# Optimization experiments

Measured on AMD Instinct MI355X. Metric: run time of the kernel, lower is better.

Reference implementation:

```python
import jax, jax.numpy as jnp
import numpy as np

SIGMA = 0.4  # init kwarg: width of Gaussian band around diagonal


def setup_inputs() -> dict:
    key = jax.random.key(0)
    k1, k2, k3 = jax.random.split(key, 3)
    B, T_OUT, T_IN = 64, 2000, 512
    alignments = jax.random.uniform(k1, (B, T_OUT, T_IN), dtype=jnp.float32)
    # lengths in [T/2, T] to avoid degenerate zero-length sequences
    input_lengths = jax.random.randint(k2, (B,), T_IN // 2, T_IN + 1, dtype=jnp.int32)
    output_lengths = jax.random.randint(k3, (B,), T_OUT // 2, T_OUT + 1, dtype=jnp.int32)
    return {"alignments": alignments, "input_lengths": input_lengths,
            "output_lengths": output_lengths}


def reference(alignments, input_lengths, output_lengths):
    B, T_out, T_in = alignments.shape
    dt = alignments.dtype
    i = jnp.arange(T_out, dtype=dt)[None, :, None]          # [1, T_out, 1]
    j = jnp.arange(T_in, dtype=dt)[None, None, :]           # [1, 1, T_in]
    Ti = input_lengths.astype(dt)[:, None, None]            # [B, 1, 1]
    To = output_lengths.astype(dt)[:, None, None]           # [B, 1, 1]
    expected_j = j / Ti * To                                # diagonal target position
    w = 1.0 - jnp.exp(-((i - expected_j) ** 2) / (2.0 * SIGMA ** 2))
    # original loops only fill b,i<T_out[b], j<T_in[b]; rest stays zero
    valid = (i < To) & (j < Ti)
    w = jnp.where(valid, w, jnp.zeros((), dt))
    return jnp.sum(alignments * w) / B
```

## Files before the change

### kernel.cpp

```cpp
#include <hip/hip_runtime.h>


#define GAL_SIGMA 0.4f
#define GAL_TIN   512
#define GAL_BMAX  256

typedef float vfloat4 __attribute__((ext_vector_type(4)));

__global__ __launch_bounds__(256) void gal_main_kernel(
    const float* __restrict__ align,
    const int*   __restrict__ in_len,
    const int*   __restrict__ out_len,
    float*       __restrict__ partials,
    int n_rows, int T_out, int B)
{
    const int lane = threadIdx.x & 63;
    const int wid  = threadIdx.x >> 6;
    const int waves_total = gridDim.x << 2;
    const float cexp = -1.0f / (2.0f * GAL_SIGMA * GAL_SIGMA);

    __shared__ int   sTo[GAL_BMAX];
    __shared__ int   sTi[GAL_BMAX];
    __shared__ float sRatio[GAL_BMAX];
    for (int t = threadIdx.x; t < B && t < GAL_BMAX; t += 256) {
        const int ti = in_len[t];
        const int to = out_len[t];
        sTi[t] = ti; sTo[t] = to;
        sRatio[t] = (float)to / (float)ti;
    }
    __syncthreads();

    float acc = 0.0f;

    const int j0a = lane << 2;
    const int j0b = 256 + (lane << 2);

    for (int row = (blockIdx.x << 2) + wid; row < n_rows; row += waves_total) {
        const int b = row / T_out;
        const int i = row - b * T_out;
        const int To = (b < GAL_BMAX) ? sTo[b] : out_len[b];
        if (i >= To) continue;
        const int   Ti    = (b < GAL_BMAX) ? sTi[b]    : in_len[b];
        const float ratio = (b < GAL_BMAX) ? sRatio[b] : ((float)To / (float)Ti);
        const float fi    = (float)i;

        const vfloat4* rowp = (const vfloat4*)(align + (size_t)row * GAL_TIN);

        const bool v0 = j0a < Ti;
        const bool v1 = j0b < Ti;
        vfloat4 a0 = {0.f, 0.f, 0.f, 0.f}, a1 = {0.f, 0.f, 0.f, 0.f};
        if (v0) a0 = __builtin_nontemporal_load(rowp + lane);
        if (v1) a1 = __builtin_nontemporal_load(rowp + lane + 64);

        if (v0) {
            #pragma unroll
            for (int e = 0; e < 4; ++e) {
                const int j = j0a + e;
                const float d = fi - (float)j * ratio;
                const float w = 1.0f - __expf(d * d * cexp);
                acc += (j < Ti) ? a0[e] * w : 0.0f;
            }
        }
        if (v1) {
            #pragma unroll
            for (int e = 0; e < 4; ++e) {
                const int j = j0b + e;
                const float d = fi - (float)j * ratio;
                const float w = 1.0f - __expf(d * d * cexp);
                acc += (j < Ti) ? a1[e] * w : 0.0f;
            }
        }
    }

    #pragma unroll
    for (int off = 32; off > 0; off >>= 1)
        acc += __shfl_down(acc, off, 64);

    __shared__ float smem[4];
    if (lane == 0) smem[wid] = acc;
    __syncthreads();
    if (threadIdx.x == 0)
        partials[blockIdx.x] = smem[0] + smem[1] + smem[2] + smem[3];
}

__global__ __launch_bounds__(256) void gal_reduce_kernel(
    const float* __restrict__ partials,
    float*       __restrict__ out,
    int n, float inv_B)
{
    float acc = 0.0f;
    for (int idx = threadIdx.x; idx < n; idx += 256)
        acc += partials[idx];

    #pragma unroll
    for (int off = 32; off > 0; off >>= 1)
        acc += __shfl_down(acc, off, 64);

    __shared__ float smem[4];
    const int lane = threadIdx.x & 63;
    const int wid  = threadIdx.x >> 6;
    if (lane == 0) smem[wid] = acc;
    __syncthreads();
    if (threadIdx.x == 0)
        out[0] = (smem[0] + smem[1] + smem[2] + smem[3]) * inv_B;
}

extern "C" void kernel_launch(void* const* d_in, const int* in_sizes, int n_in,
                              void* d_out, int out_size, void* d_ws, size_t ws_size,
                              hipStream_t stream) {
    const float* align   = (const float*)d_in[0];
    const int*   in_len  = (const int*)d_in[1];
    const int*   out_len = (const int*)d_in[2];
    float* out = (float*)d_out;
    float* partials = (float*)d_ws;

    const int B      = in_sizes[1];
    const int T_out  = in_sizes[0] / (B * GAL_TIN);
    const int n_rows = B * T_out;

    int nblocks = 4096;
    const int max_blocks = (int)(ws_size / sizeof(float));
    if (nblocks > max_blocks) nblocks = max_blocks;

    gal_main_kernel<<<nblocks, 256, 0, stream>>>(align, in_len, out_len,
                                                 partials, n_rows, T_out, B);
    gal_reduce_kernel<<<1, 256, 0, stream>>>(partials, out, nblocks, 1.0f / (float)B);
}
```

Measured before the change: 313.9 us.

## Tile grid by batch and row chunk, hoist per-column terms, prefetch next row

Replaces the flat grid-stride over all rows with a 2D grid, one block per (batch, row chunk), and clamps each chunk to the batch's output length. Rows past To are no longer visited at all, and the per-row division and length lookups go away. The per-lane j*ratio values and validity masks are hoisted out of the row loop. The next row's loads are issued before computing the current row to overlap memory latency. The grid becomes 32*B blocks, so work per block is uneven because the valid row count differs by batch, and the launch is smaller than the previous 4096 blocks.

```diff
diff --git a/kernel.cpp b/kernel.cpp
--- a/kernel.cpp
+++ b/kernel.cpp
@@ -1,9 +1,9 @@
 #include <hip/hip_runtime.h>
 
 
-#define GAL_SIGMA 0.4f
-#define GAL_TIN   512
-#define GAL_BMAX  256
+#define GAL_SIGMA  0.4f
+#define GAL_TIN    512
+#define GAL_CHUNKS 32
 
 typedef float vfloat4 __attribute__((ext_vector_type(4)));
 
@@ -12,63 +12,75 @@
     const int*   __restrict__ in_len,
     const int*   __restrict__ out_len,
     float*       __restrict__ partials,
-    int n_rows, int T_out, int B)
+    int T_out)
 {
-    const int lane = threadIdx.x & 63;
-    const int wid  = threadIdx.x >> 6;
-    const int waves_total = gridDim.x << 2;
-    const float cexp = -1.0f / (2.0f * GAL_SIGMA * GAL_SIGMA);
+    const int lane    = threadIdx.x & 63;
+    const int wid     = threadIdx.x >> 6;
+    const int b       = blockIdx.y;
+    const int nchunks = gridDim.x;
 
-    __shared__ int   sTo[GAL_BMAX];
-    __shared__ int   sTi[GAL_BMAX];
-    __shared__ float sRatio[GAL_BMAX];
-    for (int t = threadIdx.x; t < B && t < GAL_BMAX; t += 256) {
-        const int ti = in_len[t];
-        const int to = out_len[t];
-        sTi[t] = ti; sTo[t] = to;
-        sRatio[t] = (float)to / (float)ti;
-    }
-    __syncthreads();
+    const int   Ti    = in_len[b];
+    const int   To    = out_len[b];
+    const float ratio = (float)To / (float)Ti;
+    const float cexp  = -1.0f / (2.0f * GAL_SIGMA * GAL_SIGMA);
+
+    const int chunk_len = (T_out + nchunks - 1) / nchunks;
+    const int i_begin   = blockIdx.x * chunk_len;
+    int i_end = i_begin + chunk_len;
+    if (i_end > T_out) i_end = T_out;
+    if (i_end > To)    i_end = To;
 
     float acc = 0.0f;
 
-    const int j0a = lane << 2;
-    const int j0b = 256 + (lane << 2);
+    const int i0 = i_begin + wid;
+    if (i0 < i_end) {
+        const int nk = (i_end - i0 + 3) >> 2;
 
-    for (int row = (blockIdx.x << 2) + wid; row < n_rows; row += waves_total) {
-        const int b = row / T_out;
-        const int i = row - b * T_out;
-        const int To = (b < GAL_BMAX) ? sTo[b] : out_len[b];
-        if (i >= To) continue;
-        const int   Ti    = (b < GAL_BMAX) ? sTi[b]    : in_len[b];
-        const float ratio = (b < GAL_BMAX) ? sRatio[b] : ((float)To / (float)Ti);
-        const float fi    = (float)i;
+        const int ja = lane << 2;
+        const int jb = 256 + (lane << 2);
 
-        const vfloat4* rowp = (const vfloat4*)(align + (size_t)row * GAL_TIN);
+        float jra[4], jrb[4];
+        bool  mva[4], mvb[4];
+        #pragma unroll
+        for (int e = 0; e < 4; ++e) {
+            jra[e] = (float)(ja + e) * ratio;
+            jrb[e] = (float)(jb + e) * ratio;
+            mva[e] = (ja + e) < Ti;
+            mvb[e] = (jb + e) < Ti;
+        }
+        const bool v0 = ja < Ti;
+        const bool v1 = jb < Ti;
 
-        const bool v0 = j0a < Ti;
-        const bool v1 = j0b < Ti;
+        const vfloat4* p = (const vfloat4*)(align + (size_t)(b * T_out + i0) * GAL_TIN);
+
         vfloat4 a0 = {0.f, 0.f, 0.f, 0.f}, a1 = {0.f, 0.f, 0.f, 0.f};
-        if (v0) a0 = __builtin_nontemporal_load(rowp + lane);
-        if (v1) a1 = __builtin_nontemporal_load(rowp + lane + 64);
+        if (v0) a0 = __builtin_nontemporal_load(p + lane);
+        if (v1) a1 = __builtin_nontemporal_load(p + 64 + lane);
 
-        if (v0) {
+        float fi = (float)i0;
+        for (int k = 0; k < nk; ++k) {
+            vfloat4 n0 = {0.f, 0.f, 0.f, 0.f}, n1 = {0.f, 0.f, 0.f, 0.f};
+            if (k + 1 < nk) {
+                const vfloat4* pn = p + (size_t)(k + 1) * (4 * (GAL_TIN / 4));
+                if (v0) n0 = __builtin_nontemporal_load(pn + lane);
+                if (v1) n1 = __builtin_nontemporal_load(pn + 64 + lane);
+            }
+
             #pragma unroll
             for (int e = 0; e < 4; ++e) {
-                const int j = j0a + e;
-                const float d = fi - (float)j * ratio;
+                const float d = fi - jra[e];
                 const float w = 1.0f - __expf(d * d * cexp);
-                acc += (j < Ti) ? a0[e] * w : 0.0f;
+                acc += mva[e] ? a0[e] * w : 0.0f;
             }
-        }
-        if (v1) {
             #pragma unroll
             for (int e = 0; e < 4; ++e) {
-                const int j = j0b + e;
-                const float d = fi - (float)j * ratio;
+                const float d = fi - jrb[e];
                 const float w = 1.0f - __expf(d * d * cexp);
-                acc += (j < Ti) ? a1[e] * w : 0.0f;
+                acc += mvb[e] ? a1[e] * w : 0.0f;
             }
+
+            a0 = n0; a1 = n1;
+            fi += 4.0f;
         }
     }
 
@@ -80,7 +92,7 @@
     if (lane == 0) smem[wid] = acc;
     __syncthreads();
     if (threadIdx.x == 0)
-        partials[blockIdx.x] = smem[0] + smem[1] + smem[2] + smem[3];
+        partials[blockIdx.y * nchunks + blockIdx.x] = smem[0] + smem[1] + smem[2] + smem[3];
 }
 
 __global__ __launch_bounds__(256) void gal_reduce_kernel(
@@ -111,18 +123,18 @@
     const float* align   = (const float*)d_in[0];
     const int*   in_len  = (const int*)d_in[1];
     const int*   out_len = (const int*)d_in[2];
-    float* out = (float*)d_out;
+    float* out      = (float*)d_out;
     float* partials = (float*)d_ws;
 
-    const int B      = in_sizes[1];
-    const int T_out  = in_sizes[0] / (B * GAL_TIN);
-    const int n_rows = B * T_out;
+    const int B     = in_sizes[1];
+    const int T_out = in_sizes[0] / (B * GAL_TIN);
 
-    int nblocks = 4096;
-    const int max_blocks = (int)(ws_size / sizeof(float));
-    if (nblocks > max_blocks) nblocks = max_blocks;
+    int chunks = GAL_CHUNKS;
+    const int max_parts = (int)(ws_size / sizeof(float));
+    while (chunks > 1 && chunks * B > max_parts) chunks >>= 1;
 
-    gal_main_kernel<<<nblocks, 256, 0, stream>>>(align, in_len, out_len,
-                                                 partials, n_rows, T_out, B);
-    gal_reduce_kernel<<<1, 256, 0, stream>>>(partials, out, nblocks, 1.0f / (float)B);
+    gal_main_kernel<<<dim3(chunks, B), 256, 0, stream>>>(align, in_len, out_len,
+                                                         partials, T_out);
+    gal_reduce_kernel<<<1, 256, 0, stream>>>(partials, out, chunks * B,
+                                             1.0f / (float)B);
 }
```

After: 321.6 us, median of 2. 1.02x slower.
